# Kernel tuning notes

Hardware: AMD Instinct MI355X
Metric: run time of the kernel (lower is better)

The kernel has to match this reference:

```python
import jax, jax.numpy as jnp
import numpy as np

N_Q = 8        # qubits
DENC = 3       # encoding entangling layers
DVAR = 3       # variational entangling layers
SEQ = 64
BATCH = 256
D_FEAT = N_Q * (DENC + 2)   # 40, per-token feature dim
D_W = N_Q * (DVAR + 2)      # 40, per-position weight dim


def _rx(t):
    c = jnp.cos(t / 2).astype(jnp.complex64)
    s = (-1j * jnp.sin(t / 2)).astype(jnp.complex64)
    return jnp.stack([jnp.stack([c, s]), jnp.stack([s, c])])


def _ry(t):
    c = jnp.cos(t / 2)
    s = jnp.sin(t / 2)
    return jnp.stack([jnp.stack([c, -s]), jnp.stack([s, c])]).astype(jnp.complex64)


def _apply1(state, U, wire):
    # state: (2,)*N_Q complex; apply 2x2 gate on `wire`
    s = jnp.tensordot(U, state, axes=([1], [wire]))
    return jnp.moveaxis(s, 0, wire)


def _cnot(state, c, t):
    s0 = jnp.take(state, 0, axis=c)
    s1 = jnpp_flip = jnp.take(state, 1, axis=c)
    t2 = t - 1 if t > c else t
    s1 = jnp.flip(s1, axis=t2)  # X on target when control=1
    return jnp.stack([s0, s1], axis=c)


def _circuit(x, w, sign):
    # x: [D_FEAT] encoding angles, w: [D_W] variational angles
    state = jnp.zeros((2,) * N_Q, jnp.complex64).at[(0,) * N_Q].set(1.0)
    idx = 0
    for j in range(N_Q):
        state = _apply1(state, _rx(x[idx]), j)
        state = _apply1(state, _ry(x[idx + 1]), j)
        idx += 2
    for _ in range(DENC):
        for j in range(N_Q):
            state = _cnot(state, j, (j + 1) % N_Q)
        for j in range(N_Q):
            state = _apply1(state, _ry(x[idx]), j)
            idx += 1
    idx = 0
    for j in range(N_Q):
        state = _apply1(state, _rx(w[idx]), j)
        state = _apply1(state, _ry(w[idx + 1]), j)
        idx += 2
    for _ in range(DVAR):
        for j in range(N_Q):
            state = _cnot(state, j, (j + 1) % N_Q)
        for j in range(N_Q):
            state = _apply1(state, _ry(w[idx]), j)
            idx += 1
    probs = (jnp.abs(state) ** 2).astype(jnp.float32)
    return jnp.sum(probs * sign)


# observable sign tables
_Z0 = jnp.array([1.0, -1.0], jnp.float32).reshape((2,) + (1,) * (N_Q - 1))
_ZALL = jnp.array([1.0, -1.0], jnp.float32)
for _ in range(N_Q - 1):
    _ZALL = _ZALL[..., None] * jnp.array([1.0, -1.0], jnp.float32)


def _batched(sign):
    f = lambda xx, ww: _circuit(xx, ww, sign)
    f = jax.vmap(f, in_axes=(0, 0))      # over seq positions (per-position weights)
    return jax.vmap(f, in_axes=(0, None))  # over batch


_qk = _batched(_Z0)
_v = _batched(_ZALL)  # random_op fixed deterministically to Z x Z x ... x Z


def setup_inputs() -> dict:
    key = jax.random.key(0)
    k1, k2, k3, k4 = jax.random.split(key, 4)
    scale = np.float32(np.pi / 4)
    x = jax.random.normal(k1, (BATCH, SEQ, D_FEAT), jnp.float32)
    pQ = scale * (2 * jax.random.normal(k2, (SEQ, D_W), jnp.float32) - 1)
    pK = scale * (2 * jax.random.normal(k3, (SEQ, D_W), jnp.float32) - 1)
    pV = scale * (2 * jax.random.normal(k4, (SEQ, D_W), jnp.float32) - 1)
    return {"x": x, "params_Q": pQ, "params_K": pK, "params_V": pV}


def reference(x, params_Q, params_K, params_V):
    # Per-token quantum circuit sims -> scalar Q, K, V expectations
    Q = _qk(x, params_Q)   # [B, S]
    K = _qk(x, params_K)   # [B, S]
    V = _v(x, params_V)    # [B, S]  (original returns d identical copies of this)
    # Gaussian-kernel attention: alpha[b,i,m] = exp(-(Q_i - K_m)^2)
    alpha = jnp.exp(-(Q[:, :, None] - K[:, None, :]) ** 2)   # [B, S, S]
    w = alpha / jnp.sum(alpha, axis=-1, keepdims=True)
    att = jnp.einsum('bim,bm->bi', w, V)                     # [B, S]
    return x + att[:, :, None]  # broadcast over d (V copies are identical)
```

## Files before the change

kernel.cpp:

```cpp
#include <hip/hip_runtime.h>

#define SEQd 64
#define BATCHd 256
#define DF 40

typedef float f2 __attribute__((ext_vector_type(2)));
typedef __fp16 h2v __attribute__((ext_vector_type(2)));


__device__ __forceinline__ f2 mkf2(float a, float b) { f2 r; r.x = a; r.y = b; return r; }

template<int LM>
__device__ __forceinline__ float xch1(float v) {
  if constexpr (LM == 0) {
    return v;
  } else if constexpr (LM == 1 || LM == 2 || LM == 3 || LM == 7) {
    constexpr int ctrl = (LM == 1) ? 0xB1 : (LM == 2) ? 0x4E : (LM == 3) ? 0x1B
                       : 0x141;
    return __int_as_float(__builtin_amdgcn_mov_dpp(__float_as_int(v), ctrl, 0xF, 0xF, true));
  } else {
    return __int_as_float(__builtin_amdgcn_ds_swizzle(__float_as_int(v), (LM << 10) | 0x1F));
  }
}

template<int LM>
__device__ __forceinline__ f2 xch2(f2 v) {
  if constexpr (LM == 0) return v;
  f2 r; r.x = xch1<LM>(v.x); r.y = xch1<LM>(v.y); return r;
}

__device__ __forceinline__ f2 pkmul(f2 a, f2 b) {
  f2 d;
  asm("v_pk_mul_f32 %0, %1, %2" : "=v"(d) : "v"(a), "v"(b));
  return d;
}
template<bool NEGB, bool SWAPA>
__device__ __forceinline__ f2 pkfma(f2 a, f2 b, f2 c) {
  f2 d;
  if constexpr (!NEGB && !SWAPA)
    asm("v_pk_fma_f32 %0, %1, %2, %3" : "=v"(d) : "v"(a), "v"(b), "v"(c));
  else if constexpr (NEGB && !SWAPA)
    asm("v_pk_fma_f32 %0, %1, %2, %3 neg_lo:[0,1,0] neg_hi:[0,1,0]"
        : "=v"(d) : "v"(a), "v"(b), "v"(c));
  else if constexpr (!NEGB && SWAPA)
    asm("v_pk_fma_f32 %0, %1, %2, %3 op_sel:[1,0,0] op_sel_hi:[0,1,1]"
        : "=v"(d) : "v"(a), "v"(b), "v"(c));
  else
    asm("v_pk_fma_f32 %0, %1, %2, %3 op_sel:[1,0,0] op_sel_hi:[0,1,1] neg_lo:[0,1,0] neg_hi:[0,1,0]"
        : "=v"(d) : "v"(a), "v"(b), "v"(c));
  return d;
}

__device__ __forceinline__ f2 cmul(f2 a, f2 b) {
  f2 r; r.x = a.x * b.x - a.y * b.y; r.y = a.x * b.y + a.y * b.x; return r;
}
__device__ __forceinline__ f2 uget(float4 f, bool bit) {
  f2 r; r.x = bit ? f.z : f.x; r.y = bit ? -f.w : f.y; return r;
}

template<int M, int SM, int J>
__device__ __forceinline__ void ry_rec(f2* rr, f2* ii, f2 CC, f2 TV) {
  if constexpr (J < 16) {
    constexpr int LM = M & 7, RM = M >> 3;
    constexpr int RJ = RM >> 1;
    constexpr bool R0 = (RM & 1) != 0;
    constexpr int JP = J ^ RJ;
    if constexpr (JP >= J) {
      constexpr int SRj = (SM >> 3) >> 1;
      constexpr bool PJ = (__builtin_popcount(J & SRj) & 1) != 0;
      if constexpr (JP == J) {
        const f2 br = xch2<LM>(rr[J]);
        const f2 bi = xch2<LM>(ii[J]);
        rr[J] = pkfma<PJ, R0>(br, TV, pkmul(rr[J], CC));
        ii[J] = pkfma<PJ, R0>(bi, TV, pkmul(ii[J], CC));
      } else {
        constexpr bool PJP = (__builtin_popcount(JP & SRj) & 1) != 0;
        const f2 br0 = xch2<LM>(rr[JP]);
        const f2 bi0 = xch2<LM>(ii[JP]);
        const f2 br1 = xch2<LM>(rr[J]);
        const f2 bi1 = xch2<LM>(ii[J]);
        rr[J]  = pkfma<PJ,  R0>(br0, TV, pkmul(rr[J],  CC));
        ii[J]  = pkfma<PJ,  R0>(bi0, TV, pkmul(ii[J],  CC));
        rr[JP] = pkfma<PJP, R0>(br1, TV, pkmul(rr[JP], CC));
        ii[JP] = pkfma<PJP, R0>(bi1, TV, pkmul(ii[JP], CC));
      }
    }
    ry_rec<M, SM, J + 1>(rr, ii, CC, TV);
  }
}

template<int M, int SM>
__device__ __forceinline__ void ry32s(f2* rr, f2* ii, f2 cs, int lam) {
  constexpr int SL = SM & 7;
  constexpr bool S0v = ((SM >> 3) & 1) != 0;
  float t0;
  if constexpr (SL != 0) t0 = (__popc(lam & SL) & 1) ? cs.y : -cs.y;
  else                   t0 = -cs.y;
  const f2 CC = mkf2(cs.x, cs.x);
  const f2 TV = mkf2(t0, S0v ? -t0 : t0);
  ry_rec<M, SM, 0>(rr, ii, CC, TV);
}

template<int M, int SM, int J>
__device__ __forceinline__ void su2_rec(f2* rr, f2* ii, f2 QX, f2 QW, f2 SC, f2 SB) {
  if constexpr (J < 16) {
    constexpr int LM = M & 7, RM = M >> 3;
    constexpr int RJ = RM >> 1;
    constexpr bool R0 = (RM & 1) != 0;
    constexpr int JP = J ^ RJ;
    if constexpr (JP >= J) {
      constexpr int SRj = (SM >> 3) >> 1;
      constexpr bool PJ = (__builtin_popcount(J & SRj) & 1) != 0;
      if constexpr (JP == J) {
        const f2 br = xch2<LM>(rr[J]);
        const f2 bi = xch2<LM>(ii[J]);
        f2 t = pkmul(rr[J], QX);
        t = pkfma<!PJ, R0>(br, SC, t);
        t = pkfma<!PJ, false>(ii[J], SB, t);
        t = pkfma<false, R0>(bi, QW, t);
        f2 u = pkmul(ii[J], QX);
        u = pkfma<!PJ, R0>(bi, SC, u);
        u = pkfma<PJ, false>(rr[J], SB, u);
        u = pkfma<true, R0>(br, QW, u);
        rr[J] = t; ii[J] = u;
      } else {
        constexpr bool PJP = (__builtin_popcount(JP & SRj) & 1) != 0;
        const f2 br0 = xch2<LM>(rr[JP]);
        const f2 bi0 = xch2<LM>(ii[JP]);
        const f2 br1 = xch2<LM>(rr[J]);
        const f2 bi1 = xch2<LM>(ii[J]);
        f2 t0v = pkmul(rr[J], QX);
        t0v = pkfma<!PJ, R0>(br0, SC, t0v);
        t0v = pkfma<!PJ, false>(ii[J], SB, t0v);
        t0v = pkfma<false, R0>(bi0, QW, t0v);
        f2 u0v = pkmul(ii[J], QX);
        u0v = pkfma<!PJ, R0>(bi0, SC, u0v);
        u0v = pkfma<PJ, false>(rr[J], SB, u0v);
        u0v = pkfma<true, R0>(br0, QW, u0v);
        f2 t1v = pkmul(rr[JP], QX);
        t1v = pkfma<!PJP, R0>(br1, SC, t1v);
        t1v = pkfma<!PJP, false>(ii[JP], SB, t1v);
        t1v = pkfma<false, R0>(bi1, QW, t1v);
        f2 u1v = pkmul(ii[JP], QX);
        u1v = pkfma<!PJP, R0>(bi1, SC, u1v);
        u1v = pkfma<PJP, false>(rr[JP], SB, u1v);
        u1v = pkfma<true, R0>(br1, QW, u1v);
        rr[J] = t0v; ii[J] = u0v; rr[JP] = t1v; ii[JP] = u1v;
      }
    }
    su2_rec<M, SM, J + 1>(rr, ii, QX, QW, SC, SB);
  }
}

template<int M, int SM>
__device__ __forceinline__ void su2g(f2* rr, f2* ii, float4 q, int lam) {
  constexpr int SL = SM & 7;
  constexpr bool S0v = ((SM >> 3) & 1) != 0;
  float sb, sc;
  if constexpr (SL != 0) {
    const bool p = (__popc(lam & SL) & 1) != 0;
    sb = p ? -q.y : q.y; sc = p ? -q.z : q.z;
  } else { sb = q.y; sc = q.z; }
  const f2 QX = mkf2(q.x, q.x), QW = mkf2(q.w, q.w);
  const f2 SCv = mkf2(sc, S0v ? -sc : sc);
  const f2 SBv = mkf2(sb, S0v ? -sb : sb);
  su2_rec<M, SM, 0>(rr, ii, QX, QW, SCv, SBv);
}

__device__ __forceinline__ void layers32s(f2* rr, f2* ii, const f2* L, int lam) {
  ry32s<0xC0,0x7F>(rr, ii, L[0],  lam);
  ry32s<0x60,0xC0>(rr, ii, L[1],  lam);
  ry32s<0x30,0xE0>(rr, ii, L[2],  lam);
  ry32s<0x18,0xF0>(rr, ii, L[3],  lam);
  ry32s<0x0C,0xF8>(rr, ii, L[4],  lam);
  ry32s<0x06,0xFC>(rr, ii, L[5],  lam);
  ry32s<0x03,0xFE>(rr, ii, L[6],  lam);
  ry32s<0xC1,0xFF>(rr, ii, L[7],  lam);
  ry32s<0xA0,0xD5>(rr, ii, L[8],  lam);
  ry32s<0x50,0xBF>(rr, ii, L[9],  lam);
  ry32s<0x28,0x5F>(rr, ii, L[10], lam);
  ry32s<0x14,0xAF>(rr, ii, L[11], lam);
  ry32s<0x0A,0x57>(rr, ii, L[12], lam);
  ry32s<0x05,0xAB>(rr, ii, L[13], lam);
  ry32s<0xC2,0x55>(rr, ii, L[14], lam);
  ry32s<0x61,0xAA>(rr, ii, L[15], lam);
  ry32s<0xF0,0x4C>(rr, ii, L[16], lam);
  ry32s<0x78,0x6A>(rr, ii, L[17], lam);
  ry32s<0x3C,0x35>(rr, ii, L[18], lam);
  ry32s<0x1E,0x9A>(rr, ii, L[19], lam);
  ry32s<0x0F,0xCD>(rr, ii, L[20], lam);
  ry32s<0xC7,0x66>(rr, ii, L[21], lam);
  ry32s<0xA3,0x33>(rr, ii, L[22], lam);
  ry32s<0x91,0x99>(rr, ii, L[23], lam);
}

__device__ __forceinline__ void initial32s(f2* rr, f2* ii, const float4* F, int lam) {
  su2g<0x80,0x80>(rr, ii, F[0], lam);
  su2g<0x40,0x40>(rr, ii, F[1], lam);
  su2g<0x20,0x20>(rr, ii, F[2], lam);
  su2g<0x10,0x10>(rr, ii, F[3], lam);
  su2g<0x08,0x08>(rr, ii, F[4], lam);
  su2g<0x04,0x04>(rr, ii, F[5], lam);
  su2g<0x02,0x02>(rr, ii, F[6], lam);
  su2g<0x01,0x01>(rr, ii, F[7], lam);
}

__device__ __forceinline__ void pinit32s(f2* rr, f2* ii, const float4* F, int lam) {
  f2 c = mkf2(1.f, 0.f);
#pragma unroll
  for (int i = 0; i < 3; ++i)
    c = cmul(c, uget(F[7 - i], ((lam >> i) & 1) != 0));
  f2 wlo[4], whi[8];
#pragma unroll
  for (int t = 0; t < 4; ++t)
    wlo[t] = cmul(uget(F[4], (t & 1) != 0), uget(F[3], ((t >> 1) & 1) != 0));
#pragma unroll
  for (int t = 0; t < 8; ++t)
    whi[t] = cmul(cmul(uget(F[2], (t & 1) != 0), uget(F[1], ((t >> 1) & 1) != 0)),
                  uget(F[0], ((t >> 2) & 1) != 0));
#pragma unroll
  for (int k = 0; k < 32; ++k) {
    const f2 a = cmul(cmul(c, wlo[k & 3]), whi[k >> 2]);
    rr[k >> 1][k & 1] = a.x;
    ii[k >> 1][k & 1] = a.y;
  }
}

__device__ __forceinline__ uint32_t packh(float a, float b) {
  h2v h = __builtin_amdgcn_cvt_pkrtz(a, b);
  return __builtin_bit_cast(uint32_t, h);
}
__device__ __forceinline__ f2 unpackh(uint32_t u) {
  h2v h = __builtin_bit_cast(h2v, u);
  f2 r; r.x = (float)h[0]; r.y = (float)h[1]; return r;
}

__device__ __forceinline__ int snap_tgt_lane(int lam) {
  int tgt = 0;
  if (lam & 1) tgt ^= 0x2B;
  if (lam & 2) tgt ^= 0x56;
  if (lam & 4) tgt ^= 0xAC;
  return tgt;
}
__device__ __forceinline__ int snap_rck(int k) {
  return ((k & 1) ? 0xD9 : 0) ^ ((k & 2) ? 0x33 : 0) ^ ((k & 4) ? 0x66 : 0)
       ^ ((k & 8) ? 0xCC : 0) ^ ((k & 16) ? 0x19 : 0);
}

__device__ __forceinline__ void snap_write_s(const f2* rr, const f2* ii, uint32_t* sn, int lam) {
  const int tgt = snap_tgt_lane(lam);
#pragma unroll
  for (int k = 0; k < 32; ++k) {
    const int qq = tgt ^ snap_rck(k);
    sn[(qq & 7) * 36 + (qq >> 3)] = packh(rr[k >> 1][k & 1], ii[k >> 1][k & 1]);
  }
}

__device__ __forceinline__ void snap_read_s(f2* rr, f2* ii, const uint32_t* sn, int lam) {
  const uint4* p = (const uint4*)(sn + lam * 36);
#pragma unroll
  for (int t = 0; t < 8; ++t) {
    const uint4 w = p[t];
    const f2 a0 = unpackh(w.x), a1 = unpackh(w.y), a2 = unpackh(w.z), a3 = unpackh(w.w);
    rr[2 * t]     = mkf2(a0.x, a1.x);  ii[2 * t]     = mkf2(a0.y, a1.y);
    rr[2 * t + 1] = mkf2(a2.x, a3.x);  ii[2 * t + 1] = mkf2(a2.y, a3.y);
  }
}

template<int SM>
__device__ __forceinline__ float expect32s(const f2* rr, const f2* ii, int lam) {
  constexpr int SL = SM & 7, SR = SM >> 3;
  constexpr int SRj = SR >> 1;
  constexpr bool S0v = (SR & 1) != 0;
  float d = 0.f;
#pragma unroll
  for (int j = 0; j < 16; ++j) {
    const f2 pp = pkfma<false, false>(ii[j], ii[j], pkmul(rr[j], rr[j]));
    float contrib;
    if constexpr (S0v) contrib = pp.x - pp.y;
    else               contrib = pp.x + pp.y;
    const bool pj = (__builtin_popcount(j & SRj) & 1) != 0;
    d += pj ? -contrib : contrib;
  }
  float v;
  if constexpr (SL != 0) v = (__popc(lam & SL) & 1) ? -d : d;
  else                   v = d;
  v += xch1<1>(v); v += xch1<2>(v); v += xch1<4>(v);
  return v;
}

__global__ __launch_bounds__(256) void prep_var(
    const float* __restrict__ pQ, const float* __restrict__ pK,
    const float* __restrict__ pV, float* __restrict__ vtab)
{
  const int t = blockIdx.x * 256 + threadIdx.x;
  if (t >= SEQd * 3 * 32) return;
  const int slot = t & 31;
  const int sh = t >> 5;
  const int h = sh % 3, sp = sh / 3;
  const float* w = ((h == 0) ? pQ : (h == 1) ? pK : pV) + sp * DF;
  float* o = vtab + sh * 80;
  if (slot < 8) {
    float cx, sx, cy, sy;
    __sincosf(w[2 * slot]     * 0.5f, &sx, &cx);
    __sincosf(w[2 * slot + 1] * 0.5f, &sy, &cy);
    ((float4*)o)[slot] = make_float4(cy * cx, sy * sx, sy * cx, cy * sx);
  } else {
    float sn, cn;
    __sincosf(w[16 + (slot - 8)] * 0.5f, &sn, &cn);
    ((float2*)(o + 32))[slot - 8] = make_float2(cn, sn);
  }
}

__global__ __launch_bounds__(256, 3) void qsal_mono(
    const float* __restrict__ x, const float* __restrict__ vtab,
    float* __restrict__ Qo, float* __restrict__ Ko, float* __restrict__ Vo)
{
  __shared__ __align__(16) float etab[32][84];
  __shared__ __align__(16) uint32_t snap[32][296];
  __shared__ __align__(16) float vtabs[240];
  const int tid = threadIdx.x;
  const int wid = tid >> 6, lane = tid & 63;
  const int lam = lane & 7;
  const int cig = (wid << 3) | (lane >> 3);
  const int s = blockIdx.x & 63;
  const int bbase = (blockIdx.x >> 6) << 5;

  for (int t = tid; t < 1280; t += 256) {
    const int cc = t / 40, idx = t - cc * 40;
    const float ang = x[((size_t)(bbase + cc) * 64 + s) * 40 + idx];
    float sn, cn; __sincosf(ang * 0.5f, &sn, &cn);
    if (idx < 16) {
      const int wire = idx >> 1, isy = idx & 1;
      etab[cc][wire * 4 + isy * 2 + 0] = cn;
      etab[cc][wire * 4 + isy * 2 + 1] = sn;
    } else {
      etab[cc][32 + (idx - 16) * 2 + 0] = cn;
      etab[cc][32 + (idx - 16) * 2 + 1] = sn;
    }
  }
  if (tid < 60) ((float4*)vtabs)[tid] = ((const float4*)(vtab + s * 240))[tid];
  __syncthreads();
  {
    const int cc = tid >> 3, wire = tid & 7;
    float4* qt = (float4*)etab[cc];
    const float4 f = qt[wire];
    qt[wire] = make_float4(f.z * f.x, f.w * f.y, f.w * f.x, f.z * f.y);
  }
  __syncthreads();

  f2 rr[16], ii[16];
#pragma unroll 1
  for (int ph = 0; ph < 4; ++ph) {
    const f2* L;
    if (ph == 0) {
      pinit32s(rr, ii, (const float4*)etab[cig], lam);
      L = (const f2*)(etab[cig] + 32);
    } else {
      snap_read_s(rr, ii, snap[cig], lam);
      const float* th = vtabs + (ph - 1) * 80;
      initial32s(rr, ii, (const float4*)th, lam);
      L = (const f2*)(th + 32);
    }
    layers32s(rr, ii, L, lam);
    if (ph == 0) {
      snap_write_s(rr, ii, snap[cig], lam);
    } else {
      const float e = (ph == 3) ? expect32s<0x88>(rr, ii, lam)
                                : expect32s<0x4C>(rr, ii, lam);
      if (lam == 0) {
        float* op = (ph == 1) ? Qo : (ph == 2) ? Ko : Vo;
        op[(bbase + cig) * 64 + s] = e;
      }
    }
    __syncthreads();
  }
}

__global__ __launch_bounds__(256) void qsal_attn(
    const float* __restrict__ x,
    const float* __restrict__ Qv,
    const float* __restrict__ Kv,
    const float* __restrict__ Vv,
    float* __restrict__ out)
{
  const int tid  = threadIdx.x;
  const int wid  = tid >> 6;
  const int lane = tid & 63;
  const int bi   = blockIdx.x * 4 + wid;
  const int b    = bi >> 6;

  const float q = Qv[bi];
  const float k = Kv[b * 64 + lane];
  const float v = Vv[b * 64 + lane];
  const float d = q - k;
  float e  = __expf(-d * d);
  float ev = e * v;
#pragma unroll
  for (int m = 1; m < 64; m <<= 1) {
    e  += __shfl_xor(e,  m, 64);
    ev += __shfl_xor(ev, m, 64);
  }
  const float att = ev / e;

  const size_t row = (size_t)bi * DF;
  if (lane < DF) out[row + lane] = x[row + lane] + att;
}

extern "C" void kernel_launch(void* const* d_in, const int* in_sizes, int n_in,
                              void* d_out, int out_size, void* d_ws, size_t ws_size,
                              hipStream_t stream) {
  const float* x  = (const float*)d_in[0];
  const float* pQ = (const float*)d_in[1];
  const float* pK = (const float*)d_in[2];
  const float* pV = (const float*)d_in[3];
  float* out = (float*)d_out;

  const int NC = BATCHd * SEQd;
  float* Qv   = (float*)d_ws;
  float* Kv   = Qv + NC;
  float* Vv   = Kv + NC;
  float* vtab = Vv + NC;

  prep_var<<<dim3(24), dim3(256), 0, stream>>>(pQ, pK, pV, vtab);
  qsal_mono<<<dim3(512), dim3(256), 0, stream>>>(x, vtab, Qv, Kv, Vv);
  qsal_attn<<<dim3(NC / 4), dim3(256), 0, stream>>>(x, Qv, Kv, Vv, out);
}
```

Before: 77.90 us.

## Split each 8-qubit state across 16 lanes instead of 8

Each circuit state of 256 amplitudes is now distributed over 16 lanes with 16 amplitudes per lane, instead of 8 lanes with 32 amplitudes each. The gate bit mapping, lane exchanges (new DPP/swizzle combinations for more lane masks), init, snapshot layout and expectation reduction are all reworked for this split, and the grid doubles to 1024 blocks. The goal is more parallelism and fewer registers per thread, which should raise occupancy. The trade-off is more cross-lane exchange instructions per gate. The per-phase __syncthreads is also removed, which relies on each group only reading the snapshot it wrote itself.

```diff
diff --git a/kernel.cpp b/kernel.cpp
--- a/kernel.cpp
+++ b/kernel.cpp
@@ -14,10 +14,17 @@
 __device__ __forceinline__ float xch1(float v) {
   if constexpr (LM == 0) {
     return v;
-  } else if constexpr (LM == 1 || LM == 2 || LM == 3 || LM == 7) {
+  } else if constexpr (LM == 1 || LM == 2 || LM == 3 || LM == 7 || LM == 15) {
     constexpr int ctrl = (LM == 1) ? 0xB1 : (LM == 2) ? 0x4E : (LM == 3) ? 0x1B
-                       : 0x141;
+                       : (LM == 7) ? 0x141 : 0x140;
     return __int_as_float(__builtin_amdgcn_mov_dpp(__float_as_int(v), ctrl, 0xF, 0xF, true));
+  } else if constexpr (LM == 4)  { return xch1<7>(xch1<3>(v));
+  } else if constexpr (LM == 5)  { return xch1<7>(xch1<2>(v));
+  } else if constexpr (LM == 6)  { return xch1<7>(xch1<1>(v));
+  } else if constexpr (LM == 8)  { return xch1<15>(xch1<7>(v));
+  } else if constexpr (LM == 12) { return xch1<15>(xch1<3>(v));
+  } else if constexpr (LM == 13) { return xch1<15>(xch1<2>(v));
+  } else if constexpr (LM == 14) { return xch1<15>(xch1<1>(v));
   } else {
     return __int_as_float(__builtin_amdgcn_ds_swizzle(__float_as_int(v), (LM << 10) | 0x1F));
   }
@@ -60,13 +67,13 @@
 
 template<int M, int SM, int J>
 __device__ __forceinline__ void ry_rec(f2* rr, f2* ii, f2 CC, f2 TV) {
-  if constexpr (J < 16) {
-    constexpr int LM = M & 7, RM = M >> 3;
+  if constexpr (J < 8) {
+    constexpr int LM = M >> 4, RM = M & 15;
     constexpr int RJ = RM >> 1;
     constexpr bool R0 = (RM & 1) != 0;
     constexpr int JP = J ^ RJ;
     if constexpr (JP >= J) {
-      constexpr int SRj = (SM >> 3) >> 1;
+      constexpr int SRj = (SM & 15) >> 1;
       constexpr bool PJ = (__builtin_popcount(J & SRj) & 1) != 0;
       if constexpr (JP == J) {
         const f2 br = xch2<LM>(rr[J]);
@@ -90,9 +97,9 @@
 }
 
 template<int M, int SM>
-__device__ __forceinline__ void ry32s(f2* rr, f2* ii, f2 cs, int lam) {
-  constexpr int SL = SM & 7;
-  constexpr bool S0v = ((SM >> 3) & 1) != 0;
+__device__ __forceinline__ void ry16s(f2* rr, f2* ii, f2 cs, int lam) {
+  constexpr int SL = SM >> 4;
+  constexpr bool S0v = (SM & 1) != 0;
   float t0;
   if constexpr (SL != 0) t0 = (__popc(lam & SL) & 1) ? cs.y : -cs.y;
   else                   t0 = -cs.y;
@@ -103,13 +110,13 @@
 
 template<int M, int SM, int J>
 __device__ __forceinline__ void su2_rec(f2* rr, f2* ii, f2 QX, f2 QW, f2 SC, f2 SB) {
-  if constexpr (J < 16) {
-    constexpr int LM = M & 7, RM = M >> 3;
+  if constexpr (J < 8) {
+    constexpr int LM = M >> 4, RM = M & 15;
     constexpr int RJ = RM >> 1;
     constexpr bool R0 = (RM & 1) != 0;
     constexpr int JP = J ^ RJ;
     if constexpr (JP >= J) {
-      constexpr int SRj = (SM >> 3) >> 1;
+      constexpr int SRj = (SM & 15) >> 1;
       constexpr bool PJ = (__builtin_popcount(J & SRj) & 1) != 0;
       if constexpr (JP == J) {
         const f2 br = xch2<LM>(rr[J]);
@@ -154,8 +161,8 @@
 
 template<int M, int SM>
 __device__ __forceinline__ void su2g(f2* rr, f2* ii, float4 q, int lam) {
-  constexpr int SL = SM & 7;
-  constexpr bool S0v = ((SM >> 3) & 1) != 0;
+  constexpr int SL = SM >> 4;
+  constexpr bool S0v = (SM & 1) != 0;
   float sb, sc;
   if constexpr (SL != 0) {
     const bool p = (__popc(lam & SL) & 1) != 0;
@@ -167,34 +174,34 @@
   su2_rec<M, SM, 0>(rr, ii, QX, QW, SCv, SBv);
 }
 
-__device__ __forceinline__ void layers32s(f2* rr, f2* ii, const f2* L, int lam) {
-  ry32s<0xC0,0x7F>(rr, ii, L[0],  lam);
-  ry32s<0x60,0xC0>(rr, ii, L[1],  lam);
-  ry32s<0x30,0xE0>(rr, ii, L[2],  lam);
-  ry32s<0x18,0xF0>(rr, ii, L[3],  lam);
-  ry32s<0x0C,0xF8>(rr, ii, L[4],  lam);
-  ry32s<0x06,0xFC>(rr, ii, L[5],  lam);
-  ry32s<0x03,0xFE>(rr, ii, L[6],  lam);
-  ry32s<0xC1,0xFF>(rr, ii, L[7],  lam);
-  ry32s<0xA0,0xD5>(rr, ii, L[8],  lam);
-  ry32s<0x50,0xBF>(rr, ii, L[9],  lam);
-  ry32s<0x28,0x5F>(rr, ii, L[10], lam);
-  ry32s<0x14,0xAF>(rr, ii, L[11], lam);
-  ry32s<0x0A,0x57>(rr, ii, L[12], lam);
-  ry32s<0x05,0xAB>(rr, ii, L[13], lam);
-  ry32s<0xC2,0x55>(rr, ii, L[14], lam);
-  ry32s<0x61,0xAA>(rr, ii, L[15], lam);
-  ry32s<0xF0,0x4C>(rr, ii, L[16], lam);
-  ry32s<0x78,0x6A>(rr, ii, L[17], lam);
-  ry32s<0x3C,0x35>(rr, ii, L[18], lam);
-  ry32s<0x1E,0x9A>(rr, ii, L[19], lam);
-  ry32s<0x0F,0xCD>(rr, ii, L[20], lam);
-  ry32s<0xC7,0x66>(rr, ii, L[21], lam);
-  ry32s<0xA3,0x33>(rr, ii, L[22], lam);
-  ry32s<0x91,0x99>(rr, ii, L[23], lam);
-}
-
-__device__ __forceinline__ void initial32s(f2* rr, f2* ii, const float4* F, int lam) {
+__device__ __forceinline__ void layers16s(f2* rr, f2* ii, const f2* L, int lam) {
+  ry16s<0xC0,0x7F>(rr, ii, L[0],  lam);
+  ry16s<0x60,0xC0>(rr, ii, L[1],  lam);
+  ry16s<0x30,0xE0>(rr, ii, L[2],  lam);
+  ry16s<0x18,0xF0>(rr, ii, L[3],  lam);
+  ry16s<0x0C,0xF8>(rr, ii, L[4],  lam);
+  ry16s<0x06,0xFC>(rr, ii, L[5],  lam);
+  ry16s<0x03,0xFE>(rr, ii, L[6],  lam);
+  ry16s<0xC1,0xFF>(rr, ii, L[7],  lam);
+  ry16s<0xA0,0xD5>(rr, ii, L[8],  lam);
+  ry16s<0x50,0xBF>(rr, ii, L[9],  lam);
+  ry16s<0x28,0x5F>(rr, ii, L[10], lam);
+  ry16s<0x14,0xAF>(rr, ii, L[11], lam);
+  ry16s<0x0A,0x57>(rr, ii, L[12], lam);
+  ry16s<0x05,0xAB>(rr, ii, L[13], lam);
+  ry16s<0xC2,0x55>(rr, ii, L[14], lam);
+  ry16s<0x61,0xAA>(rr, ii, L[15], lam);
+  ry16s<0xF0,0x4C>(rr, ii, L[16], lam);
+  ry16s<0x78,0x6A>(rr, ii, L[17], lam);
+  ry16s<0x3C,0x35>(rr, ii, L[18], lam);
+  ry16s<0x1E,0x9A>(rr, ii, L[19], lam);
+  ry16s<0x0F,0xCD>(rr, ii, L[20], lam);
+  ry16s<0xC7,0x66>(rr, ii, L[21], lam);
+  ry16s<0xA3,0x33>(rr, ii, L[22], lam);
+  ry16s<0x91,0x99>(rr, ii, L[23], lam);
+}
+
+__device__ __forceinline__ void initial16s(f2* rr, f2* ii, const float4* F, int lam) {
   su2g<0x80,0x80>(rr, ii, F[0], lam);
   su2g<0x40,0x40>(rr, ii, F[1], lam);
   su2g<0x20,0x20>(rr, ii, F[2], lam);
@@ -205,22 +212,22 @@
   su2g<0x01,0x01>(rr, ii, F[7], lam);
 }
 
-__device__ __forceinline__ void pinit32s(f2* rr, f2* ii, const float4* F, int lam) {
+__device__ __forceinline__ void pinit16s(f2* rr, f2* ii, const float4* F, int lam) {
   f2 c = mkf2(1.f, 0.f);
 #pragma unroll
-  for (int i = 0; i < 3; ++i)
-    c = cmul(c, uget(F[7 - i], ((lam >> i) & 1) != 0));
-  f2 wlo[4], whi[8];
-#pragma unroll
-  for (int t = 0; t < 4; ++t)
-    wlo[t] = cmul(uget(F[4], (t & 1) != 0), uget(F[3], ((t >> 1) & 1) != 0));
-#pragma unroll
-  for (int t = 0; t < 8; ++t)
-    whi[t] = cmul(cmul(uget(F[2], (t & 1) != 0), uget(F[1], ((t >> 1) & 1) != 0)),
-                  uget(F[0], ((t >> 2) & 1) != 0));
-#pragma unroll
-  for (int k = 0; k < 32; ++k) {
-    const f2 a = cmul(cmul(c, wlo[k & 3]), whi[k >> 2]);
+  for (int i = 0; i < 4; ++i)
+    c = cmul(c, uget(F[3 - i], ((lam >> i) & 1) != 0));
+  f2 w67[4], w45[4];
+#pragma unroll
+  for (int j = 0; j < 4; ++j) {
+    w67[j] = cmul(uget(F[6], (j & 2) != 0), uget(F[7], (j & 1) != 0));
+    w45[j] = cmul(uget(F[4], (j & 2) != 0), uget(F[5], (j & 1) != 0));
+  }
+#pragma unroll
+  for (int k = 0; k < 16; ++k) {
+    const f2 u = w67[k & 3], w = w45[(k >> 2) & 3];
+    f2 t = cmul(u, w);
+    const f2 a = cmul(c, t);
     rr[k >> 1][k & 1] = a.x;
     ii[k >> 1][k & 1] = a.y;
   }
@@ -235,31 +242,25 @@
   f2 r; r.x = (float)h[0]; r.y = (float)h[1]; return r;
 }
 
-__device__ __forceinline__ int snap_tgt_lane(int lam) {
+__device__ __forceinline__ void snap_write16s(const f2* rr, const f2* ii,
+                                              uint32_t* sn, int lam) {
   int tgt = 0;
-  if (lam & 1) tgt ^= 0x2B;
-  if (lam & 2) tgt ^= 0x56;
-  if (lam & 4) tgt ^= 0xAC;
-  return tgt;
-}
-__device__ __forceinline__ int snap_rck(int k) {
-  return ((k & 1) ? 0xD9 : 0) ^ ((k & 2) ? 0x33 : 0) ^ ((k & 4) ? 0x66 : 0)
-       ^ ((k & 8) ? 0xCC : 0) ^ ((k & 16) ? 0x19 : 0);
-}
-
-__device__ __forceinline__ void snap_write_s(const f2* rr, const f2* ii, uint32_t* sn, int lam) {
-  const int tgt = snap_tgt_lane(lam);
-#pragma unroll
-  for (int k = 0; k < 32; ++k) {
-    const int qq = tgt ^ snap_rck(k);
-    sn[(qq & 7) * 36 + (qq >> 3)] = packh(rr[k >> 1][k & 1], ii[k >> 1][k & 1]);
-  }
-}
-
-__device__ __forceinline__ void snap_read_s(f2* rr, f2* ii, const uint32_t* sn, int lam) {
-  const uint4* p = (const uint4*)(sn + lam * 36);
-#pragma unroll
-  for (int t = 0; t < 8; ++t) {
+  if (lam & 1) tgt ^= 0x33;
+  if (lam & 2) tgt ^= 0x66;
+  if (lam & 4) tgt ^= 0xCC;
+  if (lam & 8) tgt ^= 0x19;
+#pragma unroll
+  for (int k = 0; k < 16; ++k) {
+    const int rck = ((k & 1) ? 0x2B : 0) ^ ((k & 2) ? 0x56 : 0)
+                  ^ ((k & 4) ? 0xAC : 0) ^ ((k & 8) ? 0xD9 : 0);
+    sn[tgt ^ rck] = packh(rr[k >> 1][k & 1], ii[k >> 1][k & 1]);
+  }
+}
+
+__device__ __forceinline__ void snap_read16s(f2* rr, f2* ii, const uint32_t* sn, int lam) {
+  const uint4* p = (const uint4*)(sn + lam * 16);
+#pragma unroll
+  for (int t = 0; t < 4; ++t) {
     const uint4 w = p[t];
     const f2 a0 = unpackh(w.x), a1 = unpackh(w.y), a2 = unpackh(w.z), a3 = unpackh(w.w);
     rr[2 * t]     = mkf2(a0.x, a1.x);  ii[2 * t]     = mkf2(a0.y, a1.y);
@@ -268,13 +269,13 @@
 }
 
 template<int SM>
-__device__ __forceinline__ float expect32s(const f2* rr, const f2* ii, int lam) {
-  constexpr int SL = SM & 7, SR = SM >> 3;
-  constexpr int SRj = SR >> 1;
-  constexpr bool S0v = (SR & 1) != 0;
+__device__ __forceinline__ float expect16s(const f2* rr, const f2* ii, int lam) {
+  constexpr int SL = SM >> 4, SR4 = SM & 15;
+  constexpr int SRj = SR4 >> 1;
+  constexpr bool S0v = (SR4 & 1) != 0;
   float d = 0.f;
 #pragma unroll
-  for (int j = 0; j < 16; ++j) {
+  for (int j = 0; j < 8; ++j) {
     const f2 pp = pkfma<false, false>(ii[j], ii[j], pkmul(rr[j], rr[j]));
     float contrib;
     if constexpr (S0v) contrib = pp.x - pp.y;
@@ -285,7 +286,7 @@
   float v;
   if constexpr (SL != 0) v = (__popc(lam & SL) & 1) ? -d : d;
   else                   v = d;
-  v += xch1<1>(v); v += xch1<2>(v); v += xch1<4>(v);
+  v += xch1<1>(v); v += xch1<2>(v); v += xch1<4>(v); v += xch1<8>(v);
   return v;
 }
 
@@ -316,17 +317,17 @@
     const float* __restrict__ x, const float* __restrict__ vtab,
     float* __restrict__ Qo, float* __restrict__ Ko, float* __restrict__ Vo)
 {
-  __shared__ __align__(16) float etab[32][84];
-  __shared__ __align__(16) uint32_t snap[32][296];
+  __shared__ __align__(16) float etab[16][84];
+  __shared__ __align__(16) uint32_t snap[16][264];
   __shared__ __align__(16) float vtabs[240];
   const int tid = threadIdx.x;
   const int wid = tid >> 6, lane = tid & 63;
-  const int lam = lane & 7;
-  const int cig = (wid << 3) | (lane >> 3);
+  const int lam = lane & 15;
+  const int cig = (wid << 2) | (lane >> 4);
   const int s = blockIdx.x & 63;
-  const int bbase = (blockIdx.x >> 6) << 5;
-
-  for (int t = tid; t < 1280; t += 256) {
+  const int bbase = (blockIdx.x >> 6) << 4;
+
+  for (int t = tid; t < 640; t += 256) {
     const int cc = t / 40, idx = t - cc * 40;
     const float ang = x[((size_t)(bbase + cc) * 64 + s) * 40 + idx];
     float sn, cn; __sincosf(ang * 0.5f, &sn, &cn);
@@ -341,7 +342,7 @@
   }
   if (tid < 60) ((float4*)vtabs)[tid] = ((const float4*)(vtab + s * 240))[tid];
   __syncthreads();
-  {
+  if (tid < 128) {
     const int cc = tid >> 3, wire = tid & 7;
     float4* qt = (float4*)etab[cc];
     const float4 f = qt[wire];
@@ -349,31 +350,30 @@
   }
   __syncthreads();
 
-  f2 rr[16], ii[16];
+  f2 rr[8], ii[8];
 #pragma unroll 1
   for (int ph = 0; ph < 4; ++ph) {
     const f2* L;
     if (ph == 0) {
-      pinit32s(rr, ii, (const float4*)etab[cig], lam);
+      pinit16s(rr, ii, (const float4*)etab[cig], lam);
       L = (const f2*)(etab[cig] + 32);
     } else {
-      snap_read_s(rr, ii, snap[cig], lam);
+      snap_read16s(rr, ii, snap[cig], lam);
       const float* th = vtabs + (ph - 1) * 80;
-      initial32s(rr, ii, (const float4*)th, lam);
+      initial16s(rr, ii, (const float4*)th, lam);
       L = (const f2*)(th + 32);
     }
-    layers32s(rr, ii, L, lam);
+    layers16s(rr, ii, L, lam);
     if (ph == 0) {
-      snap_write_s(rr, ii, snap[cig], lam);
+      snap_write16s(rr, ii, snap[cig], lam);
     } else {
-      const float e = (ph == 3) ? expect32s<0x88>(rr, ii, lam)
-                                : expect32s<0x4C>(rr, ii, lam);
+      const float e = (ph == 3) ? expect16s<0x88>(rr, ii, lam)
+                                : expect16s<0x4C>(rr, ii, lam);
       if (lam == 0) {
         float* op = (ph == 1) ? Qo : (ph == 2) ? Ko : Vo;
         op[(bbase + cig) * 64 + s] = e;
       }
     }
-    __syncthreads();
   }
 }
 
@@ -423,6 +423,6 @@
   float* vtab = Vv + NC;
 
   prep_var<<<dim3(24), dim3(256), 0, stream>>>(pQ, pK, pV, vtab);
-  qsal_mono<<<dim3(512), dim3(256), 0, stream>>>(x, vtab, Qv, Kv, Vv);
+  qsal_mono<<<dim3(1024), dim3(256), 0, stream>>>(x, vtab, Qv, Kv, Vv);
   qsal_attn<<<dim3(NC / 4), dim3(256), 0, stream>>>(x, Qv, Kv, Vv, out);
 }
```

Measured after the change: 82.94 us. 1.06x slower.
